# Performance work log

Hardware: AMD Instinct MI355X
Metric: run time of the kernel (lower is better)

Reference implementation:

```python
import jax, jax.numpy as jnp
import numpy as np

BN_EPS = 1e-5
STRIDE = 12          # ACCENT_DOWNSAMPLE_STRIDE
NQ = 8               # ACCENT_VQ_QUANTIZERS
K = 256              # ACCENT_VQ_CODEBOOK_SIZE
VQ_D = 16            # ACCENT_VQ_DIM
EMB = 128            # ACCENT_EMBEDDING_DIM


def conv1d(x, w, b, stride=1, padding=0):
    # x: (B, Cin, T), w: (Cout, Cin, Kw)
    y = jax.lax.conv_general_dilated(
        x, w, window_strides=(stride,), padding=[(padding, padding)],
        dimension_numbers=("NCW", "OIW", "NCW"))
    return y + b[None, :, None]


def batchnorm(x, gamma, beta, mean, var):
    # eval-mode BatchNorm1d over channel dim
    inv = jax.lax.rsqrt(var + BN_EPS)
    return (x - mean[None, :, None]) * (inv * gamma)[None, :, None] + beta[None, :, None]


def setup_inputs() -> dict:
    key = jax.random.key(0)
    ks = jax.random.split(key, 12)
    C = 256
    d = {
        "mel_spectrogram": jax.random.normal(ks[0], (16, 80, 4096), jnp.float32),
        "w1": jax.random.normal(ks[1], (C, 80, 5), jnp.float32) * 0.05,
        "b1": jnp.zeros((C,), jnp.float32),
        "g1": jnp.ones((C,), jnp.float32),
        "be1": jnp.zeros((C,), jnp.float32),
        "m1": jax.random.normal(ks[2], (C,), jnp.float32) * 0.1,
        "v1": jax.random.uniform(ks[3], (C,), jnp.float32, 0.5, 1.5),
        "w2": jax.random.normal(ks[4], (C, C, 5), jnp.float32) * 0.03,
        "b2": jnp.zeros((C,), jnp.float32),
        "g2": jnp.ones((C,), jnp.float32),
        "be2": jnp.zeros((C,), jnp.float32),
        "m2": jax.random.normal(ks[5], (C,), jnp.float32) * 0.1,
        "v2": jax.random.uniform(ks[6], (C,), jnp.float32, 0.5, 1.5),
        "wd": jax.random.normal(ks[7], (EMB, C, 2 * STRIDE), jnp.float32) * 0.02,
        "bd": jnp.zeros((EMB,), jnp.float32),
        "wp": jax.random.normal(ks[8], (VQ_D, EMB, 1), jnp.float32) * 0.1,
        "bp": jnp.zeros((VQ_D,), jnp.float32),
        "codebooks": jax.random.normal(ks[9], (NQ, K, VQ_D), jnp.float32) * 0.3,
    }
    return d


def reference(mel_spectrogram, w1, b1, g1, be1, m1, v1,
              w2, b2, g2, be2, m2, v2, wd, bd, wp, bp, codebooks):
    # CNN stack
    x = jax.nn.relu(batchnorm(conv1d(mel_spectrogram, w1, b1, 1, 2), g1, be1, m1, v1))
    x = jax.nn.relu(batchnorm(conv1d(x, w2, b2, 1, 2), g2, be2, m2, v2))
    # Downsample conv: kernel=24, stride=12, pad=6
    e_a_unq = conv1d(x, wd, bd, STRIDE, STRIDE // 2)          # (B, 128, T')
    z = conv1d(e_a_unq, wp, bp, 1, 0)                          # (B, 16, T')
    # RVQ: 8 sequential cdist-argmin-subtract steps
    r = jnp.transpose(z, (0, 2, 1))                            # (B, T', 16)
    idx_list = []
    for q in range(NQ):
        cb = codebooks[q]                                      # (K, 16)
        # squared euclidean distances (B, T', K)
        d = (jnp.sum(r * r, -1, keepdims=True)
             - 2.0 * jnp.einsum("btd,kd->btk", r, cb)
             + jnp.sum(cb * cb, -1))
        idx = jnp.argmin(d, axis=-1)                           # (B, T')
        idx_list.append(idx)
        r = r - cb[idx]                                        # residual update
    indices = jnp.stack(idx_list, axis=0)                      # (NQ, B, T')
    return e_a_unq, indices
```

## Files before the change

kernel.cpp:

```cpp
#include <hip/hip_runtime.h>
#include <math.h>

#define B_    16
#define BCH   4
#define T_    4096
#define C_    256
#define CIN1  80
#define EMB   128
#define TP    341
#define NPOS  (B_*TP)
#define NQ_   8
#define KCB   256
#define BN_EPS 1e-5

__global__ __launch_bounds__(256) void prep_f64(
    const float* __restrict__ w1, const float* __restrict__ w2,
    const float* __restrict__ wd,
    const float* __restrict__ b1, const float* __restrict__ g1,
    const float* __restrict__ be1, const float* __restrict__ m1,
    const float* __restrict__ v1,
    const float* __restrict__ b2, const float* __restrict__ g2,
    const float* __restrict__ be2, const float* __restrict__ m2,
    const float* __restrict__ v2,
    const float* __restrict__ wp, const float* __restrict__ bp,
    double* __restrict__ w1t, double* __restrict__ w2t, double* __restrict__ wdt,
    double* __restrict__ a1, double* __restrict__ bt1,
    double* __restrict__ a2, double* __restrict__ bt2,
    double* __restrict__ wpd, double* __restrict__ bpd)
{
    int j = blockIdx.x * 256 + threadIdx.x;
    if (j < 256*24*128) wdt[j] = (double)wd[(size_t)(j & 127) * 6144 + (j >> 7)];
    if (j < 256*5*256)  w2t[j] = (double)w2[(size_t)(j & 255) * 1280 + (j >> 8)];
    if (j < 80*5*256)   w1t[j] = (double)w1[(size_t)(j & 255) * 400 + (j >> 8)];
    if (j < 16*128)     wpd[j] = (double)wp[j];
    if (j < 16)         bpd[j] = (double)bp[j];
    if (j < 256) {
        double inv1 = 1.0 / sqrt((double)v1[j] + BN_EPS);
        double s1 = (double)g1[j] * inv1;
        a1[j]  = s1;
        bt1[j] = ((double)b1[j] - (double)m1[j]) * s1 + (double)be1[j];
        double inv2 = 1.0 / sqrt((double)v2[j] + BN_EPS);
        double s2 = (double)g2[j] * inv2;
        a2[j]  = s2;
        bt2[j] = ((double)b2[j] - (double)m2[j]) * s2 + (double)be2[j];
    }
}

__device__ __forceinline__ int swz_pair(int col) {
    int bw = col >> 1;
    return ((bw ^ ((bw >> 3) & 7)) << 1);
}
__device__ __forceinline__ int swz_scalar(int col) {
    int bw = col >> 1;
    return (((bw ^ ((bw >> 3) & 7)) << 1) | (col & 1));
}

template<int CIN, typename Tin>
__global__ __launch_bounds__(256) void conv5_bn_relu_f64(
    const Tin* __restrict__ in,
    const double* __restrict__ wt,
    const double* __restrict__ alpha, const double* __restrict__ beta,
    double* __restrict__ out)
{
    const int b   = blockIdx.z;
    const int co0 = blockIdx.y * 64;
    const int t0  = blockIdx.x * 128;
    const int tid = threadIdx.x;
    const int tcol = tid & 15;
    const int trow = tid >> 4;

    __shared__ double xs[8][136];
    __shared__ double wsh[40][64];

    double acc[4][8];
    #pragma unroll
    for (int i = 0; i < 4; ++i)
        #pragma unroll
        for (int j = 0; j < 8; ++j) acc[i][j] = 0.0;

    for (int c0 = 0; c0 < CIN; c0 += 8) {
        for (int i = tid; i < 8 * 132; i += 256) {
            int ci = i / 132, col = i % 132;
            int t = t0 - 2 + col;
            double v = 0.0;
            if (t >= 0 && t < T_) v = (double)in[((size_t)(b * CIN + c0 + ci)) * T_ + t];
            xs[ci][swz_scalar(col)] = v;
        }
        for (int i = tid; i < 40 * 64; i += 256) {
            int r = i >> 6, co = i & 63;
            wsh[r][co] = wt[(size_t)(c0 * 5 + r) * 256 + co0 + co];
        }
        __syncthreads();

        #pragma unroll
        for (int ci = 0; ci < 8; ++ci) {
            double xv[12];
            #pragma unroll
            for (int m = 0; m < 6; ++m) {
                double2 v = *(const double2*)&xs[ci][swz_pair(tcol * 8 + 2 * m)];
                xv[2 * m] = v.x; xv[2 * m + 1] = v.y;
            }
            #pragma unroll
            for (int k = 0; k < 5; ++k) {
                double w0 = wsh[ci * 5 + k][trow * 4 + 0];
                double w1v = wsh[ci * 5 + k][trow * 4 + 1];
                double w2v = wsh[ci * 5 + k][trow * 4 + 2];
                double w3v = wsh[ci * 5 + k][trow * 4 + 3];
                #pragma unroll
                for (int j = 0; j < 8; ++j) {
                    double xq = xv[j + k];
                    acc[0][j] = fma(w0, xq, acc[0][j]);
                    acc[1][j] = fma(w1v, xq, acc[1][j]);
                    acc[2][j] = fma(w2v, xq, acc[2][j]);
                    acc[3][j] = fma(w3v, xq, acc[3][j]);
                }
            }
        }
        __syncthreads();
    }

    const int cobase = co0 + trow * 4;
    const int tg = t0 + tcol * 8;
    #pragma unroll
    for (int i = 0; i < 4; ++i) {
        double a = alpha[cobase + i], bt = beta[cobase + i];
        size_t base = ((size_t)(b * C_ + cobase + i)) * T_ + tg;
        #pragma unroll
        for (int j = 0; j < 8; ++j) {
            double y = fma(acc[i][j], a, bt);
            out[base + j] = y > 0.0 ? y : 0.0;
        }
    }
}

__global__ __launch_bounds__(256) void convd_f64_v5(
    const double* __restrict__ x2,
    const double* __restrict__ wdt,
    double* __restrict__ parts,
    int nb, int nsplit, int cis)
{
    const int bz  = blockIdx.z;
    const int s   = bz % nsplit;
    const int b   = bz / nsplit;
    const int co0 = blockIdx.y * 64;
    const int tp0 = blockIdx.x * 128;
    const int tid = threadIdx.x;
    const int tcol = tid & 31;
    const int crow = tid >> 5;

    __shared__ double xs[2][1552];
    __shared__ double wsh[48][64];

    double acc[8][4];
    #pragma unroll
    for (int i = 0; i < 8; ++i)
        #pragma unroll
        for (int j = 0; j < 4; ++j) acc[i][j] = 0.0;

    const int tbase = tp0 * 12 - 6;
    const int ci_begin = s * cis;

    for (int c0 = ci_begin; c0 < ci_begin + cis; c0 += 2) {
        for (int i = tid; i < 2 * 1548; i += 256) {
            int ci = i / 1548, col = i % 1548;
            int t = tbase + col;
            double v = (t >= 0 && t < T_)
                ? x2[((size_t)(b * 256 + c0 + ci)) * T_ + t] : 0.0;
            xs[ci][swz_scalar(col)] = v;
        }
        for (int i = tid; i < 48 * 64; i += 256) {
            int r = i >> 6, c = i & 63;
            wsh[r][c] = wdt[(size_t)(c0 * 24 + r) * 128 + co0 + c];
        }
        __syncthreads();

        #pragma unroll
        for (int ci = 0; ci < 2; ++ci) {
            #pragma unroll
            for (int kk = 0; kk < 12; ++kk) {
                const double* wr0 = &wsh[ci * 24 + 2 * kk][crow * 8];
                const double* wr1 = &wsh[ci * 24 + 2 * kk + 1][crow * 8];
                double2 xp[4];
                #pragma unroll
                for (int j = 0; j < 4; ++j) {
                    int bw = (tcol + 32 * j) * 6 + kk;
                    int colp = ((bw ^ ((bw >> 3) & 7)) << 1);
                    xp[j] = *(const double2*)&xs[ci][colp];
                }
                #pragma unroll
                for (int i = 0; i < 8; ++i) {
                    double wa = wr0[i], wb = wr1[i];
                    #pragma unroll
                    for (int j = 0; j < 4; ++j) {
                        acc[i][j] = fma(wa, xp[j].x, acc[i][j]);
                        acc[i][j] = fma(wb, xp[j].y, acc[i][j]);
                    }
                }
            }
        }
        __syncthreads();
    }

    #pragma unroll
    for (int i = 0; i < 8; ++i) {
        int co = co0 + crow * 8 + i;
        #pragma unroll
        for (int j = 0; j < 4; ++j) {
            int tp = tp0 + tcol + 32 * j;
            if (tp < TP)
                parts[(((size_t)s * nb + b) * EMB + co) * TP + tp] = acc[i][j];
        }
    }
}

__global__ __launch_bounds__(256) void convd_combine(
    const double* __restrict__ parts,
    const float* __restrict__ bd,
    double* __restrict__ ed,
    float* __restrict__ e_out,
    int nb, int b_off, int nsplit)
{
    int idx = blockIdx.x * 256 + threadIdx.x;
    int total = nb * EMB * TP;
    if (idx >= total) return;
    int b_local = idx / (EMB * TP);
    int rem = idx % (EMB * TP);
    int co = rem / TP;
    size_t stride = (size_t)nb * EMB * TP;
    double y = 0.0;
    for (int s = 0; s < nsplit; ++s)
        y += parts[(size_t)s * stride + idx];
    y += (double)bd[co];
    size_t o = (size_t)(b_off + b_local) * EMB * TP + rem;
    ed[o] = y;
    e_out[o] = (float)y;
}

__global__ __launch_bounds__(128) void zproj_f64(
    const double* __restrict__ ed,
    const double* __restrict__ wpd,
    const double* __restrict__ bpd,
    double* __restrict__ z)
{
    const int b = blockIdx.y;
    const int t = blockIdx.x * 128 + threadIdx.x;
    __shared__ double wps[16][128];
    for (int i = threadIdx.x; i < 16 * 128; i += 128)
        wps[i >> 7][i & 127] = wpd[i];
    __syncthreads();
    if (t >= TP) return;
    double acc[16];
    #pragma unroll
    for (int v = 0; v < 16; ++v) acc[v] = bpd[v];
    for (int co = 0; co < 128; ++co) {
        double x = ed[((size_t)(b * EMB + co)) * TP + t];
        #pragma unroll
        for (int v = 0; v < 16; ++v) acc[v] = fma(x, wps[v][co], acc[v]);
    }
    #pragma unroll
    for (int v = 0; v < 16; ++v)
        z[((size_t)(b * TP + t)) * 16 + v] = acc[v];
}

__global__ __launch_bounds__(256) void rvq_f64_v2(
    const double* __restrict__ z,
    const float* __restrict__ cb,
    float* __restrict__ out_idx)
{
    const int pos = blockIdx.x;
    const int tid = threadIdx.x;
    const int lane = tid & 63;
    const int wv = tid >> 6;

    __shared__ double r[16];
    __shared__ double wd_s[4];
    __shared__ int wi_s[4];
    __shared__ int best_s;

    if (tid < 16) r[tid] = z[(size_t)pos * 16 + tid];
    __syncthreads();

    for (int q = 0; q < NQ_; ++q) {
        const float* c = cb + ((size_t)(q * KCB) + tid) * 16;
        double d = 0.0;
        #pragma unroll
        for (int i = 0; i < 16; ++i) {
            double diff = r[i] - (double)c[i];
            d = fma(diff, diff, d);
        }
        int idx = tid;
        #pragma unroll
        for (int sft = 32; sft > 0; sft >>= 1) {
            double d2 = __shfl_down(d, sft, 64);
            int i2 = __shfl_down(idx, sft, 64);
            if (d2 < d || (d2 == d && i2 < idx)) { d = d2; idx = i2; }
        }
        if (lane == 0) { wd_s[wv] = d; wi_s[wv] = idx; }
        __syncthreads();
        if (tid == 0) {
            double bd_ = wd_s[0]; int bi = wi_s[0];
            #pragma unroll
            for (int w = 1; w < 4; ++w) {
                if (wd_s[w] < bd_ || (wd_s[w] == bd_ && wi_s[w] < bi)) {
                    bd_ = wd_s[w]; bi = wi_s[w];
                }
            }
            best_s = bi;
            out_idx[(size_t)q * NPOS + pos] = (float)bi;
        }
        __syncthreads();
        int best = best_s;
        if (tid < 16)
            r[tid] = r[tid] - (double)cb[((size_t)(q * KCB) + best) * 16 + tid];
        __syncthreads();
    }
}

extern "C" void kernel_launch(void* const* d_in, const int* in_sizes, int n_in,
                              void* d_out, int out_size, void* d_ws, size_t ws_size,
                              hipStream_t stream) {
    const float* mel = (const float*)d_in[0];
    const float* w1  = (const float*)d_in[1];
    const float* b1  = (const float*)d_in[2];
    const float* g1  = (const float*)d_in[3];
    const float* be1 = (const float*)d_in[4];
    const float* m1  = (const float*)d_in[5];
    const float* v1  = (const float*)d_in[6];
    const float* w2  = (const float*)d_in[7];
    const float* b2  = (const float*)d_in[8];
    const float* g2  = (const float*)d_in[9];
    const float* be2 = (const float*)d_in[10];
    const float* m2  = (const float*)d_in[11];
    const float* v2  = (const float*)d_in[12];
    const float* wd  = (const float*)d_in[13];
    const float* bd  = (const float*)d_in[14];
    const float* wp  = (const float*)d_in[15];
    const float* bp  = (const float*)d_in[16];
    const float* cb  = (const float*)d_in[17];

    auto need = [](int nb, int ns) -> size_t {
        size_t s = 0;
        s += (size_t)BCH * C_ * T_ * 8;
        s += (size_t)nb * C_ * T_ * 8;
        s += (size_t)80*5*256*8 + (size_t)256*5*256*8 + (size_t)256*24*128*8;
        s += 4 * 2048 + 16384 + 256;
        s += (size_t)16 * EMB * TP * 8;
        s += (size_t)16 * TP * 16 * 8;
        s += (size_t)ns * nb * EMB * TP * 8;
        s += 16384;
        return s;
    };
    int nb = 8, nsplit = 8;
    if (ws_size >= need(16, 8))      { nb = 16; nsplit = 8; }
    else if (ws_size >= need(16, 4)) { nb = 16; nsplit = 4; }
    const int ngrp = B_ / nb;
    const int cis  = 256 / nsplit;

    char* ws = (char*)d_ws;
    size_t off = 0;
    auto alloc = [&](size_t bytes) -> char* {
        char* p = ws + off;
        off = (off + bytes + 255) & ~(size_t)255;
        return p;
    };
    double* x1d  = (double*)alloc((size_t)BCH * C_ * T_ * 8);
    double* x2d  = (double*)alloc((size_t)nb * C_ * T_ * 8);
    double* w1td = (double*)alloc((size_t)80*5*256*8);
    double* w2td = (double*)alloc((size_t)256*5*256*8);
    double* wdtd = (double*)alloc((size_t)256*24*128*8);
    double* a1d  = (double*)alloc(2048);
    double* bt1d = (double*)alloc(2048);
    double* a2d  = (double*)alloc(2048);
    double* bt2d = (double*)alloc(2048);
    double* wpd  = (double*)alloc(16*128*8);
    double* bpd  = (double*)alloc(16*8);
    double* ed   = (double*)alloc((size_t)16 * EMB * TP * 8);
    double* zd   = (double*)alloc((size_t)16 * TP * 16 * 8);
    double* parts= (double*)alloc((size_t)nsplit * nb * EMB * TP * 8);

    float* e_out   = (float*)d_out;
    float* idx_out = (float*)d_out + (size_t)B_ * EMB * TP;

    prep_f64<<<3072, 256, 0, stream>>>(w1, w2, wd, b1, g1, be1, m1, v1,
                                       b2, g2, be2, m2, v2, wp, bp,
                                       w1td, w2td, wdtd, a1d, bt1d, a2d, bt2d,
                                       wpd, bpd);

    const int comb_blocks = (nb * EMB * TP + 255) / 256;
    for (int g = 0; g < ngrp; ++g) {
        for (int ch = 0; ch < nb / BCH; ++ch) {
            int ch_abs = g * (nb / BCH) + ch;
            const float* mel_c = mel + (size_t)ch_abs * BCH * CIN1 * T_;
            conv5_bn_relu_f64<CIN1, float><<<dim3(32, 4, BCH), 256, 0, stream>>>(
                mel_c, w1td, a1d, bt1d, x1d);
            conv5_bn_relu_f64<C_, double><<<dim3(32, 4, BCH), 256, 0, stream>>>(
                x1d, w2td, a2d, bt2d, x2d + (size_t)ch * BCH * C_ * T_);
        }
        convd_f64_v5<<<dim3(3, 2, nb * nsplit), 256, 0, stream>>>(
            x2d, wdtd, parts, nb, nsplit, cis);
        convd_combine<<<comb_blocks, 256, 0, stream>>>(parts, bd, ed, e_out,
                                                       nb, g * nb, nsplit);
    }
    zproj_f64<<<dim3(3, 16), 128, 0, stream>>>(ed, wpd, bpd, zd);
    rvq_f64_v2<<<NPOS, 256, 0, stream>>>(zd, cb, idx_out);
}
```

Measured before the change: 1.662 ms.

## Retile downsample conv to full 128-channel blocks with im2col-style smem layout

```diff
diff --git a/kernel.cpp b/kernel.cpp
--- a/kernel.cpp
+++ b/kernel.cpp
@@ -133,7 +133,7 @@
     }
 }
 
-__global__ __launch_bounds__(256) void convd_f64_v5(
+__global__ __launch_bounds__(256) void convd_f64_v6(
     const double* __restrict__ x2,
     const double* __restrict__ wdt,
     double* __restrict__ parts,
@@ -142,14 +142,13 @@
     const int bz  = blockIdx.z;
     const int s   = bz % nsplit;
     const int b   = bz / nsplit;
-    const int co0 = blockIdx.y * 64;
-    const int tp0 = blockIdx.x * 128;
+    const int tp0 = blockIdx.x * 64;
     const int tid = threadIdx.x;
-    const int tcol = tid & 31;
-    const int crow = tid >> 5;
-
-    __shared__ double xs[2][1552];
-    __shared__ double wsh[48][64];
+    const int tcol = tid & 15;
+    const int crow = tid >> 4;
+
+    __shared__ double xs2[2][24][66];
+    __shared__ double wsh[48][128];
 
     double acc[8][4];
     #pragma unroll
@@ -161,41 +160,37 @@
     const int ci_begin = s * cis;
 
     for (int c0 = ci_begin; c0 < ci_begin + cis; c0 += 2) {
-        for (int i = tid; i < 2 * 1548; i += 256) {
-            int ci = i / 1548, col = i % 1548;
-            int t = tbase + col;
+        for (int i = tid; i < 2 * 780; i += 256) {
+            int ci = i / 780, c = i % 780;
+            int t = tbase + c;
             double v = (t >= 0 && t < T_)
                 ? x2[((size_t)(b * 256 + c0 + ci)) * T_ + t] : 0.0;
-            xs[ci][swz_scalar(col)] = v;
-        }
-        for (int i = tid; i < 48 * 64; i += 256) {
-            int r = i >> 6, c = i & 63;
-            wsh[r][c] = wdt[(size_t)(c0 * 24 + r) * 128 + co0 + c];
-        }
-        __syncthreads();
-
+            int tp = c / 12, kp = c % 12;
+            xs2[ci][kp][tp] = v;
+            if (tp >= 1) xs2[ci][kp + 12][tp - 1] = v;
+        }
+        for (int i = tid; i < 48 * 128; i += 256) {
+            int r = i >> 7, c = i & 127;
+            wsh[r][c] = wdt[(size_t)(c0 * 24 + r) * 128 + c];
+        }
+        __syncthreads();
+
+        const double* xb = &xs2[0][0][0] + tcol;
+        const double* wb = &wsh[0][0] + crow * 8;
         #pragma unroll
         for (int ci = 0; ci < 2; ++ci) {
             #pragma unroll
-            for (int kk = 0; kk < 12; ++kk) {
-                const double* wr0 = &wsh[ci * 24 + 2 * kk][crow * 8];
-                const double* wr1 = &wsh[ci * 24 + 2 * kk + 1][crow * 8];
-                double2 xp[4];
+            for (int k = 0; k < 24; ++k) {
+                double wv[8], xv[4];
                 #pragma unroll
-                for (int j = 0; j < 4; ++j) {
-                    int bw = (tcol + 32 * j) * 6 + kk;
-                    int colp = ((bw ^ ((bw >> 3) & 7)) << 1);
-                    xp[j] = *(const double2*)&xs[ci][colp];
-                }
+                for (int i = 0; i < 8; ++i) wv[i] = wb[(ci * 24 + k) * 128 + i];
                 #pragma unroll
-                for (int i = 0; i < 8; ++i) {
-                    double wa = wr0[i], wb = wr1[i];
+                for (int j = 0; j < 4; ++j) xv[j] = xb[(ci * 24 + k) * 66 + 16 * j];
+                #pragma unroll
+                for (int i = 0; i < 8; ++i)
                     #pragma unroll
-                    for (int j = 0; j < 4; ++j) {
-                        acc[i][j] = fma(wa, xp[j].x, acc[i][j]);
-                        acc[i][j] = fma(wb, xp[j].y, acc[i][j]);
-                    }
-                }
+                    for (int j = 0; j < 4; ++j)
+                        acc[i][j] = fma(wv[i], xv[j], acc[i][j]);
             }
         }
         __syncthreads();
@@ -203,10 +198,10 @@
 
     #pragma unroll
     for (int i = 0; i < 8; ++i) {
-        int co = co0 + crow * 8 + i;
+        int co = crow * 8 + i;
         #pragma unroll
         for (int j = 0; j < 4; ++j) {
-            int tp = tp0 + tcol + 32 * j;
+            int tp = tp0 + tcol + 16 * j;
             if (tp < TP)
                 parts[(((size_t)s * nb + b) * EMB + co) * TP + tp] = acc[i][j];
         }
@@ -338,23 +333,27 @@
     const float* bp  = (const float*)d_in[16];
     const float* cb  = (const float*)d_in[17];
 
-    auto need = [](int nb, int ns) -> size_t {
-        size_t s = 0;
-        s += (size_t)BCH * C_ * T_ * 8;
-        s += (size_t)nb * C_ * T_ * 8;
-        s += (size_t)80*5*256*8 + (size_t)256*5*256*8 + (size_t)256*24*128*8;
-        s += 4 * 2048 + 16384 + 256;
-        s += (size_t)16 * EMB * TP * 8;
-        s += (size_t)16 * TP * 16 * 8;
-        s += (size_t)ns * nb * EMB * TP * 8;
-        s += 16384;
-        return s;
+    const int nb = 8;
+    const int ngrp = B_ / nb;
+
+    const size_t x1_bytes    = (size_t)BCH * C_ * T_ * 8;
+    const size_t x2_bytes    = (size_t)nb * C_ * T_ * 8;
+    const size_t fixed_bytes = x2_bytes + (size_t)80*5*256*8 + (size_t)256*5*256*8
+                             + (size_t)256*24*128*8 + 4*2048 + 16384 + 256
+                             + (size_t)16 * EMB * TP * 8
+                             + (size_t)16 * TP * 16 * 8
+                             + 16384;
+    auto parts_bytes = [&](int ns) -> size_t {
+        return (size_t)ns * nb * EMB * TP * 8;
     };
-    int nb = 8, nsplit = 8;
-    if (ws_size >= need(16, 8))      { nb = 16; nsplit = 8; }
-    else if (ws_size >= need(16, 4)) { nb = 16; nsplit = 4; }
-    const int ngrp = B_ / nb;
-    const int cis  = 256 / nsplit;
+    auto need = [&](int ns) -> size_t {
+        size_t shared = x1_bytes > parts_bytes(ns) ? x1_bytes : parts_bytes(ns);
+        return shared + fixed_bytes;
+    };
+    int nsplit = (ws_size >= need(16)) ? 16 : 8;
+    const int cis = 256 / nsplit;
+    const size_t shared_bytes =
+        x1_bytes > parts_bytes(nsplit) ? x1_bytes : parts_bytes(nsplit);
 
     char* ws = (char*)d_ws;
     size_t off = 0;
@@ -363,8 +362,10 @@
         off = (off + bytes + 255) & ~(size_t)255;
         return p;
     };
-    double* x1d  = (double*)alloc((size_t)BCH * C_ * T_ * 8);
-    double* x2d  = (double*)alloc((size_t)nb * C_ * T_ * 8);
+    char* shared = alloc(shared_bytes);
+    double* x1d  = (double*)shared;
+    double* parts= (double*)shared;
+    double* x2d  = (double*)alloc(x2_bytes);
     double* w1td = (double*)alloc((size_t)80*5*256*8);
     double* w2td = (double*)alloc((size_t)256*5*256*8);
     double* wdtd = (double*)alloc((size_t)256*24*128*8);
@@ -376,7 +377,6 @@
     double* bpd  = (double*)alloc(16*8);
     double* ed   = (double*)alloc((size_t)16 * EMB * TP * 8);
     double* zd   = (double*)alloc((size_t)16 * TP * 16 * 8);
-    double* parts= (double*)alloc((size_t)nsplit * nb * EMB * TP * 8);
 
     float* e_out   = (float*)d_out;
     float* idx_out = (float*)d_out + (size_t)B_ * EMB * TP;
@@ -396,7 +396,7 @@
             conv5_bn_relu_f64<C_, double><<<dim3(32, 4, BCH), 256, 0, stream>>>(
                 x1d, w2td, a2d, bt2d, x2d + (size_t)ch * BCH * C_ * T_);
         }
-        convd_f64_v5<<<dim3(3, 2, nb * nsplit), 256, 0, stream>>>(
+        convd_f64_v6<<<dim3(6, 1, nb * nsplit), 256, 0, stream>>>(
             x2d, wdtd, parts, nb, nsplit, cis);
         convd_combine<<<comb_blocks, 256, 0, stream>>>(parts, bd, ed, e_out,
                                                        nb, g * nb, nsplit);
```

After: 1.876 ms. +12.9%, slower.
